# Performance work log

Measured on AMD Instinct MI355X. Metric: run time of the kernel, lower is better.

## Reference

```python
import jax, jax.numpy as jnp
import numpy as np

IN_F = 4096
OUT_F = 4096
SPLIT_F = 410   # ceil(4096 * 0.1)
NUM_PARTS = 10  # ceil(4096 / 410)


def setup_inputs() -> dict:
    key = jax.random.key(0)
    ks = jax.random.split(key, 7)
    s = 1.0 / np.sqrt(IN_F)
    sn = 1.0 / np.sqrt(NUM_PARTS)
    return {
        'x': jax.random.normal(ks[0], (2, 2048, IN_F), dtype=jnp.float32),
        'Wsel': jax.random.uniform(ks[1], (NUM_PARTS, IN_F), jnp.float32, -s, s),
        'bsel': jax.random.uniform(ks[2], (NUM_PARTS,), jnp.float32, -s, s),
        'Wexp': jax.random.uniform(ks[3], (IN_F, NUM_PARTS), jnp.float32, -sn, sn),
        'bexp': jax.random.uniform(ks[4], (IN_F,), jnp.float32, -sn, sn),
        'Wfc': jax.random.uniform(ks[5], (SPLIT_F, IN_F), jnp.float32, -s, s),
        'bfc': jax.random.uniform(ks[6], (SPLIT_F,), jnp.float32, -s, s),
        'out_features': OUT_F,
    }


def reference(x, Wsel, bsel, Wexp, bexp, Wfc, bfc, out_features):
    # selector: sx[..., n]
    sx = jnp.einsum('bsi,ni->bsn', x, Wsel) + bsel
    # expander(diag_embed(sx)): px[..., n, f] = sx[..., n] * Wexp[f, n] + bexp[f]
    # (diag matrix never materialized; mathematically identical)
    px = sx[..., :, None] * Wexp.T[None, None, :, :] + bexp  # [b, s, n, in]
    xx = x[..., None, :] + px                                # broadcast-add of x
    y = jnp.einsum('bsni,fi->bsnf', xx, Wfc) + bfc           # splitfc, [b, s, n, sf]
    y = y.reshape(y.shape[0], y.shape[1], -1)                # (n sf) flatten
    return y[..., :out_features]
```

## Files before the change

### kernel.cpp

```cpp
#include <hip/hip_runtime.h>
#include <hip/hip_bf16.h>
#include <stdint.h>

#define TKS    4096
#define KD     4096
#define NSF    410
#define NPARTS 10
#define OUTF   4096

typedef unsigned short u16;
typedef __attribute__((ext_vector_type(8))) short bf16x8;
typedef __attribute__((ext_vector_type(4))) float f32x4;

#define WS_XB  0
#define WS_BSW ((size_t)TKS * KD * 2)
#define WS_SX  (WS_BSW + (size_t)448 * 512 * 8 * 2)
#define WS_GC  (WS_SX + (size_t)TKS * NPARTS * 4)

__device__ inline u16 f2bf(float f) {
    union { __hip_bfloat16 b; u16 u; } cv;
    cv.b = __float2bfloat16(f);
    return cv.u;
}

__device__ inline int g_row(int g) { int s = g >> 6; return (s >> 2) * 32 + (s & 1) * 16 + (g & 15); }
__device__ inline int g_col(int g) { int s = g >> 6; return ((s >> 1) & 1) * 32 + ((g >> 4) & 3) * 8; }

__global__ __launch_bounds__(256) void prep(const float* __restrict__ x,
                                            const float* __restrict__ Wsel,
                                            const float* __restrict__ bsel,
                                            const float* __restrict__ Wexp,
                                            const float* __restrict__ bexp,
                                            const float* __restrict__ Wfc,
                                            const float* __restrict__ bfc,
                                            u16* __restrict__ xb,
                                            u16* __restrict__ bsw,
                                            float* __restrict__ sxb,
                                            float* __restrict__ gc) {
    const int bid = blockIdx.x;
    const int tid = threadIdx.x;

    if (bid < 128) {
        const int b3 = bid;
        const int w = tid >> 6, lane = tid & 63;
        const int t0 = b3 * 32 + w * 8;
        float acc[8][NPARTS];
#pragma unroll
        for (int t = 0; t < 8; ++t)
#pragma unroll
            for (int n = 0; n < NPARTS; ++n) acc[t][n] = 0.f;

        for (int k4 = 0; k4 < 16; ++k4) {
            const int k = k4 * 256 + lane * 4;
            float4 ws[NPARTS];
#pragma unroll
            for (int n = 0; n < NPARTS; ++n)
                ws[n] = *(const float4*)&Wsel[(size_t)n * KD + k];
#pragma unroll
            for (int t = 0; t < 8; ++t) {
                float4 xv = *(const float4*)&x[(size_t)(t0 + t) * KD + k];
#pragma unroll
                for (int n = 0; n < NPARTS; ++n)
                    acc[t][n] += xv.x * ws[n].x + xv.y * ws[n].y
                               + xv.z * ws[n].z + xv.w * ws[n].w;
            }
        }
#pragma unroll
        for (int s = 1; s < 64; s <<= 1)
#pragma unroll
            for (int t = 0; t < 8; ++t)
#pragma unroll
                for (int n = 0; n < NPARTS; ++n)
                    acc[t][n] += __shfl_xor(acc[t][n], s);
        if (lane == 0) {
#pragma unroll
            for (int t = 0; t < 8; ++t)
#pragma unroll
                for (int n = 0; n < NPARTS; ++n)
                    sxb[(size_t)(t0 + t) * NPARTS + n] = acc[t][n] + bsel[n];
        }

    } else if (bid < 142) {
        const int b4 = bid - 128;
        const int w = tid >> 6, lane = tid & 63;
        const int f0 = b4 * 32 + w * 8;
        float acc[8][11];
#pragma unroll
        for (int t = 0; t < 8; ++t)
#pragma unroll
            for (int n = 0; n < 11; ++n) acc[t][n] = 0.f;

        for (int k4 = 0; k4 < 16; ++k4) {
            const int k = k4 * 256 + lane * 4;
            float we[4][11];
#pragma unroll
            for (int j = 0; j < 4; ++j) {
#pragma unroll
                for (int n = 0; n < NPARTS; ++n)
                    we[j][n] = Wexp[(size_t)(k + j) * NPARTS + n];
                we[j][10] = bexp[k + j];
            }
#pragma unroll
            for (int t = 0; t < 8; ++t) {
                const int f = f0 + t;
                float4 xv = (f < NSF) ? *(const float4*)&Wfc[(size_t)f * KD + k]
                                      : make_float4(0.f, 0.f, 0.f, 0.f);
#pragma unroll
                for (int n = 0; n < 11; ++n)
                    acc[t][n] += xv.x * we[0][n] + xv.y * we[1][n]
                               + xv.z * we[2][n] + xv.w * we[3][n];
            }
        }
#pragma unroll
        for (int s = 1; s < 64; s <<= 1)
#pragma unroll
            for (int t = 0; t < 8; ++t)
#pragma unroll
                for (int n = 0; n < 11; ++n)
                    acc[t][n] += __shfl_xor(acc[t][n], s);
        if (lane == 0) {
#pragma unroll
            for (int t = 0; t < 8; ++t) {
                const int f = f0 + t;
#pragma unroll
                for (int n = 0; n < NPARTS; ++n)
                    gc[(size_t)f * 12 + n] = (f < NSF) ? acc[t][n] : 0.f;
                gc[(size_t)f * 12 + 10] = (f < NSF) ? acc[t][10] + bfc[f] : 0.f;
            }
        }

    } else if (bid < 8334) {
        const int b1 = bid - 142;
        const int kt = b1 & 63, tb = b1 >> 6;
        const int g = tid;
        const int slot = g >> 6;
        const int row = (slot & 1) * 16 + (g & 15);
        const int col = (slot >> 1) * 32 + ((g >> 4) & 3) * 8;
        const float* src = x + (size_t)(tb * 32 + row) * KD + kt * 64 + col;
        float4 v0 = *(const float4*)src;
        float4 v1 = *(const float4*)(src + 4);
        u16 h[8] = { f2bf(v0.x), f2bf(v0.y), f2bf(v0.z), f2bf(v0.w),
                     f2bf(v1.x), f2bf(v1.y), f2bf(v1.z), f2bf(v1.w) };
        *(uint4*)&xb[((size_t)(tb * 64 + kt) * 256 + g) * 8] = *(uint4*)h;

    } else {
        const int b2 = bid - 8334;
        const int kt = b2 & 63, rb = b2 >> 6;
        u16* tout = bsw + ((size_t)(rb * 64 + kt) * 512) * 8;
#pragma unroll
        for (int j = 0; j < 2; ++j) {
            const int g = j * 256 + tid;
            const int r = rb * 64 + g_row(g);
            uint4 pk = make_uint4(0u, 0u, 0u, 0u);
            if (r < NSF) {
                const float* src = Wfc + (size_t)r * KD + kt * 64 + g_col(g);
                float4 v0 = *(const float4*)src;
                float4 v1 = *(const float4*)(src + 4);
                u16 h[8] = { f2bf(v0.x), f2bf(v0.y), f2bf(v0.z), f2bf(v0.w),
                             f2bf(v1.x), f2bf(v1.y), f2bf(v1.z), f2bf(v1.w) };
                pk = *(uint4*)h;
            }
            *(uint4*)&tout[(size_t)g * 8] = pk;
        }
    }
}

#define A_IDX(kt, mi, ks) ((((size_t)(tb * 2 + ((mi) >> 1)) * 64 + (size_t)(kt)) * 256 \
                            + ((ks) * 2 + ((mi) & 1)) * 64 + lane) * 8)
#define B_IDX(kt, nj, ks) (((size_t)(fb * 64 + (kt)) * 512 \
                            + (wf * 4 + (ks) * 2 + (nj)) * 64 + lane) * 8)

__global__ __launch_bounds__(256, 2) void main_kernel(const u16* __restrict__ xb,
                                                      const u16* __restrict__ bsw,
                                                      float* __restrict__ out) {
    __shared__ float red[4][4][16][34];

    const int tid = threadIdx.x;
    const int f2 = blockIdx.x >> 6;
    const int tb = blockIdx.x & 63;
    const int lane = tid & 63;
    const int kh = tid >> 6;
    const int q = lane >> 4, ml = lane & 15;
    const int fb = f2 >> 1, wf = f2 & 1;

    f32x4 acc[4][2];
#pragma unroll
    for (int mi = 0; mi < 4; ++mi)
#pragma unroll
        for (int nj = 0; nj < 2; ++nj) acc[mi][nj] = (f32x4){0.f,0.f,0.f,0.f};

    bf16x8 fa[4][4], fbv[4][2];

#define LOADAB(p, kt, ks) do {                                            \
        _Pragma("unroll")                                                 \
        for (int mi = 0; mi < 4; ++mi)                                    \
            fa[p][mi] = *(const bf16x8*)&xb[A_IDX((kt), mi, (ks))];       \
        _Pragma("unroll")                                                 \
        for (int nj = 0; nj < 2; ++nj)                                    \
            fbv[p][nj] = *(const bf16x8*)&bsw[B_IDX((kt), nj, (ks))];     \
    } while (0)

#define MFMAS(p) do {                                                     \
        _Pragma("unroll")                                                 \
        for (int mi = 0; mi < 4; ++mi)                                    \
            _Pragma("unroll")                                             \
            for (int nj = 0; nj < 2; ++nj)                                \
                acc[mi][nj] = __builtin_amdgcn_mfma_f32_16x16x32_bf16(    \
                    fa[p][mi], fbv[p][nj], acc[mi][nj], 0, 0, 0);         \
    } while (0)

#define LD(p, s) LOADAB((p), kh * 16 + ((s) >> 1), (s) & 1)

    LD(0, 0); LD(1, 1); LD(2, 2);
    __builtin_amdgcn_sched_group_barrier(0x020, 18, 0);
#pragma unroll
    for (int s = 0; s < 32; ++s) {
        if (s + 3 < 32) LD((s + 3) & 3, s + 3);
        MFMAS(s & 3);
        if (s + 3 < 32)
            __builtin_amdgcn_sched_group_barrier(0x020, 6, 0);
        __builtin_amdgcn_sched_group_barrier(0x008, 8, 0);
    }
#undef LD
#undef LOADAB
#undef MFMAS

#pragma unroll
    for (int mi = 0; mi < 4; ++mi)
#pragma unroll
        for (int nj = 0; nj < 2; ++nj)
#pragma unroll
            for (int r = 0; r < 4; ++r)
                red[mi][kh][q * 4 + r][nj * 16 + ml] = acc[mi][nj][r];
    __syncthreads();

#pragma unroll
    for (int nj = 0; nj < 2; ++nj) {
        const int fl = nj * 16 + ml;
        const int fg = f2 * 32 + fl;
        if (fg >= NSF) continue;
#pragma unroll
        for (int r = 0; r < 4; ++r) {
            const int tl = kh * 16 + q * 4 + r;
            const float v = red[kh][0][q * 4 + r][fl] + red[kh][1][q * 4 + r][fl]
                          + red[kh][2][q * 4 + r][fl] + red[kh][3][q * 4 + r][fl];
            out[(size_t)(tb * 64 + tl) * OUTF + fg] = v;
        }
    }
}

__global__ __launch_bounds__(256) void expand(const float* __restrict__ sxb,
                                              const float* __restrict__ gc,
                                              float* out) {
    __shared__ float Ct[4][412];
    __shared__ float sxl[4][NPARTS];
    const int tid = threadIdx.x;
    const int t0 = blockIdx.x * 4;

    int   ns[4][4], fgs[4][4];
    float gv[4][4], cv[4][4];
#pragma unroll
    for (int g = 0; g < 4; ++g)
#pragma unroll
        for (int e = 0; e < 4; ++e) {
            const int j = g * 1024 + tid * 4 + e;
            const int n = j / NSF;
            const int fg = j - n * NSF;
            ns[g][e] = n; fgs[g][e] = fg;
            gv[g][e] = gc[(size_t)fg * 12 + n];
            cv[g][e] = gc[(size_t)fg * 12 + 10];
        }

    for (int i = tid; i < 4 * NSF; i += 256)
        Ct[i / NSF][i % NSF] = out[(size_t)(t0 + i / NSF) * OUTF + (i % NSF)];
    if (tid < 4 * NPARTS)
        sxl[tid / NPARTS][tid % NPARTS] =
            sxb[(size_t)(t0 + tid / NPARTS) * NPARTS + tid % NPARTS];
    __syncthreads();

#pragma unroll
    for (int r = 0; r < 4; ++r) {
        float* orow = out + (size_t)(t0 + r) * OUTF;
#pragma unroll
        for (int g = 0; g < 4; ++g) {
            float4 v;
            v.x = Ct[r][fgs[g][0]] + sxl[r][ns[g][0]] * gv[g][0] + cv[g][0];
            v.y = Ct[r][fgs[g][1]] + sxl[r][ns[g][1]] * gv[g][1] + cv[g][1];
            v.z = Ct[r][fgs[g][2]] + sxl[r][ns[g][2]] * gv[g][2] + cv[g][2];
            v.w = Ct[r][fgs[g][3]] + sxl[r][ns[g][3]] * gv[g][3] + cv[g][3];
            *(float4*)&orow[g * 1024 + tid * 4] = v;
        }
    }
}

extern "C" void kernel_launch(void* const* d_in, const int* in_sizes, int n_in,
                              void* d_out, int out_size, void* d_ws, size_t ws_size,
                              hipStream_t stream) {
    const float* x    = (const float*)d_in[0];
    const float* Wsel = (const float*)d_in[1];
    const float* bsel = (const float*)d_in[2];
    const float* Wexp = (const float*)d_in[3];
    const float* bexp = (const float*)d_in[4];
    const float* Wfc  = (const float*)d_in[5];
    const float* bfc  = (const float*)d_in[6];
    float* out = (float*)d_out;

    char* ws = (char*)d_ws;
    u16* xb    = (u16*)(ws + WS_XB);
    u16* bsw   = (u16*)(ws + WS_BSW);
    float* sxb = (float*)(ws + WS_SX);
    float* gcv = (float*)(ws + WS_GC);

    prep<<<dim3(128 + 14 + 8192 + 448), dim3(256), 0, stream>>>(
        x, Wsel, bsel, Wexp, bexp, Wfc, bfc, xb, bsw, sxb, gcv);
    main_kernel<<<dim3(13 * 64), dim3(256), 0, stream>>>(xb, bsw, out);
    expand<<<dim3(1024), dim3(256), 0, stream>>>(sxb, gcv, out);
}
```

Baseline: 206.5 us.

## Split selector/gate reductions across K chunks with atomics into separate kernel

The long serial selector and gate-coefficient reductions, which ran as 142 blocks each looping over all of K, are split into 8 K-chunks per block group and combined with atomicAdd in a new kernel. The per-chunk results go into a buffer that the retile kernel zeroes first. The retile path now converts two K tiles per block, which halves its block count. The goal is to stop a few slow blocks from setting the tail of the prep kernel, at the cost of an extra launch, atomics and non-deterministic summation order.

New measurement: 235.4 us. 1.14x slower.

```diff
diff --git a/kernel.cpp b/kernel.cpp
--- a/kernel.cpp
+++ b/kernel.cpp
@@ -16,6 +16,7 @@
 #define WS_BSW ((size_t)TKS * KD * 2)
 #define WS_SX  (WS_BSW + (size_t)448 * 512 * 8 * 2)
 #define WS_GC  (WS_SX + (size_t)TKS * NPARTS * 4)
+#define ZERO_U4 ((TKS * NPARTS + 448 * 12) * 4 / 16)
 
 __device__ inline u16 f2bf(float f) {
     union { __hip_bfloat16 b; u16 u; } cv;
@@ -26,125 +27,34 @@
 __device__ inline int g_row(int g) { int s = g >> 6; return (s >> 2) * 32 + (s & 1) * 16 + (g & 15); }
 __device__ inline int g_col(int g) { int s = g >> 6; return ((s >> 1) & 1) * 32 + ((g >> 4) & 3) * 8; }
 
-__global__ __launch_bounds__(256) void prep(const float* __restrict__ x,
-                                            const float* __restrict__ Wsel,
-                                            const float* __restrict__ bsel,
-                                            const float* __restrict__ Wexp,
-                                            const float* __restrict__ bexp,
-                                            const float* __restrict__ Wfc,
-                                            const float* __restrict__ bfc,
-                                            u16* __restrict__ xb,
-                                            u16* __restrict__ bsw,
-                                            float* __restrict__ sxb,
-                                            float* __restrict__ gc) {
+__global__ __launch_bounds__(256) void retile(const float* __restrict__ x,
+                                              const float* __restrict__ Wfc,
+                                              u16* __restrict__ xb,
+                                              u16* __restrict__ bsw,
+                                              uint4* __restrict__ zbase) {
     const int bid = blockIdx.x;
     const int tid = threadIdx.x;
 
-    if (bid < 128) {
-        const int b3 = bid;
-        const int w = tid >> 6, lane = tid & 63;
-        const int t0 = b3 * 32 + w * 8;
-        float acc[8][NPARTS];
-#pragma unroll
-        for (int t = 0; t < 8; ++t)
-#pragma unroll
-            for (int n = 0; n < NPARTS; ++n) acc[t][n] = 0.f;
-
-        for (int k4 = 0; k4 < 16; ++k4) {
-            const int k = k4 * 256 + lane * 4;
-            float4 ws[NPARTS];
-#pragma unroll
-            for (int n = 0; n < NPARTS; ++n)
-                ws[n] = *(const float4*)&Wsel[(size_t)n * KD + k];
-#pragma unroll
-            for (int t = 0; t < 8; ++t) {
-                float4 xv = *(const float4*)&x[(size_t)(t0 + t) * KD + k];
-#pragma unroll
-                for (int n = 0; n < NPARTS; ++n)
-                    acc[t][n] += xv.x * ws[n].x + xv.y * ws[n].y
-                               + xv.z * ws[n].z + xv.w * ws[n].w;
-            }
-        }
-#pragma unroll
-        for (int s = 1; s < 64; s <<= 1)
-#pragma unroll
-            for (int t = 0; t < 8; ++t)
-#pragma unroll
-                for (int n = 0; n < NPARTS; ++n)
-                    acc[t][n] += __shfl_xor(acc[t][n], s);
-        if (lane == 0) {
-#pragma unroll
-            for (int t = 0; t < 8; ++t)
-#pragma unroll
-                for (int n = 0; n < NPARTS; ++n)
-                    sxb[(size_t)(t0 + t) * NPARTS + n] = acc[t][n] + bsel[n];
-        }
-
-    } else if (bid < 142) {
-        const int b4 = bid - 128;
-        const int w = tid >> 6, lane = tid & 63;
-        const int f0 = b4 * 32 + w * 8;
-        float acc[8][11];
-#pragma unroll
-        for (int t = 0; t < 8; ++t)
-#pragma unroll
-            for (int n = 0; n < 11; ++n) acc[t][n] = 0.f;
-
-        for (int k4 = 0; k4 < 16; ++k4) {
-            const int k = k4 * 256 + lane * 4;
-            float we[4][11];
-#pragma unroll
-            for (int j = 0; j < 4; ++j) {
-#pragma unroll
-                for (int n = 0; n < NPARTS; ++n)
-                    we[j][n] = Wexp[(size_t)(k + j) * NPARTS + n];
-                we[j][10] = bexp[k + j];
-            }
-#pragma unroll
-            for (int t = 0; t < 8; ++t) {
-                const int f = f0 + t;
-                float4 xv = (f < NSF) ? *(const float4*)&Wfc[(size_t)f * KD + k]
-                                      : make_float4(0.f, 0.f, 0.f, 0.f);
-#pragma unroll
-                for (int n = 0; n < 11; ++n)
-                    acc[t][n] += xv.x * we[0][n] + xv.y * we[1][n]
-                               + xv.z * we[2][n] + xv.w * we[3][n];
-            }
-        }
-#pragma unroll
-        for (int s = 1; s < 64; s <<= 1)
-#pragma unroll
-            for (int t = 0; t < 8; ++t)
-#pragma unroll
-                for (int n = 0; n < 11; ++n)
-                    acc[t][n] += __shfl_xor(acc[t][n], s);
-        if (lane == 0) {
-#pragma unroll
-            for (int t = 0; t < 8; ++t) {
-                const int f = f0 + t;
-#pragma unroll
-                for (int n = 0; n < NPARTS; ++n)
-                    gc[(size_t)f * 12 + n] = (f < NSF) ? acc[t][n] : 0.f;
-                gc[(size_t)f * 12 + 10] = (f < NSF) ? acc[t][10] + bfc[f] : 0.f;
-            }
-        }
-
-    } else if (bid < 8334) {
-        const int b1 = bid - 142;
-        const int kt = b1 & 63, tb = b1 >> 6;
+    if (bid < 4096) {
+        const int ktp = bid & 31, tb = bid >> 5;
         const int g = tid;
         const int slot = g >> 6;
         const int row = (slot & 1) * 16 + (g & 15);
         const int col = (slot >> 1) * 32 + ((g >> 4) & 3) * 8;
-        const float* src = x + (size_t)(tb * 32 + row) * KD + kt * 64 + col;
-        float4 v0 = *(const float4*)src;
-        float4 v1 = *(const float4*)(src + 4);
-        u16 h[8] = { f2bf(v0.x), f2bf(v0.y), f2bf(v0.z), f2bf(v0.w),
-                     f2bf(v1.x), f2bf(v1.y), f2bf(v1.z), f2bf(v1.w) };
-        *(uint4*)&xb[((size_t)(tb * 64 + kt) * 256 + g) * 8] = *(uint4*)h;
-
-    } else {
-        const int b2 = bid - 8334;
+        const float* src = x + (size_t)(tb * 32 + row) * KD + ktp * 128 + col;
+        float4 a0 = *(const float4*)src;
+        float4 a1 = *(const float4*)(src + 4);
+        float4 b0 = *(const float4*)(src + 64);
+        float4 b1 = *(const float4*)(src + 68);
+        u16 ha[8] = { f2bf(a0.x), f2bf(a0.y), f2bf(a0.z), f2bf(a0.w),
+                      f2bf(a1.x), f2bf(a1.y), f2bf(a1.z), f2bf(a1.w) };
+        u16 hb[8] = { f2bf(b0.x), f2bf(b0.y), f2bf(b0.z), f2bf(b0.w),
+                      f2bf(b1.x), f2bf(b1.y), f2bf(b1.z), f2bf(b1.w) };
+        *(uint4*)&xb[((size_t)(tb * 64 + ktp * 2 + 0) * 256 + g) * 8] = *(uint4*)ha;
+        *(uint4*)&xb[((size_t)(tb * 64 + ktp * 2 + 1) * 256 + g) * 8] = *(uint4*)hb;
+
+    } else if (bid < 4544) {
+        const int b2 = bid - 4096;
         const int kt = b2 & 63, rb = b2 >> 6;
         u16* tout = bsw + ((size_t)(rb * 64 + kt) * 512) * 8;
 #pragma unroll
@@ -162,6 +72,120 @@
             }
             *(uint4*)&tout[(size_t)g * 8] = pk;
         }
+
+    } else {
+        for (int i = tid; i < ZERO_U4; i += 256)
+            zbase[i] = make_uint4(0u, 0u, 0u, 0u);
+    }
+}
+
+__global__ __launch_bounds__(256) void selg(const float* __restrict__ x,
+                                            const float* __restrict__ Wsel,
+                                            const float* __restrict__ bsel,
+                                            const float* __restrict__ Wexp,
+                                            const float* __restrict__ bexp,
+                                            const float* __restrict__ Wfc,
+                                            const float* __restrict__ bfc,
+                                            float* __restrict__ sxb,
+                                            float* __restrict__ gc) {
+    const int bid = blockIdx.x;
+    const int tid = threadIdx.x;
+    const int w = tid >> 6, lane = tid & 63;
+
+    if (bid < 1024) {
+        const int b3 = bid >> 3, kc = bid & 7;
+        const int t0 = b3 * 32 + w * 8;
+        float acc[8][NPARTS];
+#pragma unroll
+        for (int t = 0; t < 8; ++t)
+#pragma unroll
+            for (int n = 0; n < NPARTS; ++n) acc[t][n] = 0.f;
+
+#pragma unroll
+        for (int k4 = 0; k4 < 2; ++k4) {
+            const int k = kc * 512 + k4 * 256 + lane * 4;
+            float4 ws[NPARTS];
+#pragma unroll
+            for (int n = 0; n < NPARTS; ++n)
+                ws[n] = *(const float4*)&Wsel[(size_t)n * KD + k];
+#pragma unroll
+            for (int t = 0; t < 8; ++t) {
+                float4 xv = *(const float4*)&x[(size_t)(t0 + t) * KD + k];
+#pragma unroll
+                for (int n = 0; n < NPARTS; ++n)
+                    acc[t][n] += xv.x * ws[n].x + xv.y * ws[n].y
+                               + xv.z * ws[n].z + xv.w * ws[n].w;
+            }
+        }
+#pragma unroll
+        for (int s = 1; s < 64; s <<= 1)
+#pragma unroll
+            for (int t = 0; t < 8; ++t)
+#pragma unroll
+                for (int n = 0; n < NPARTS; ++n)
+                    acc[t][n] += __shfl_xor(acc[t][n], s);
+        if (lane == 0) {
+#pragma unroll
+            for (int t = 0; t < 8; ++t)
+#pragma unroll
+                for (int n = 0; n < NPARTS; ++n) {
+                    float v = acc[t][n] + (kc == 0 ? bsel[n] : 0.f);
+                    atomicAdd(&sxb[(size_t)(t0 + t) * NPARTS + n], v);
+                }
+        }
+
+    } else {
+        const int b4 = bid - 1024;
+        const int fb = b4 >> 3, kc = b4 & 7;
+        const int f0 = fb * 32 + w * 8;
+        float acc[8][11];
+#pragma unroll
+        for (int t = 0; t < 8; ++t)
+#pragma unroll
+            for (int n = 0; n < 11; ++n) acc[t][n] = 0.f;
+
+#pragma unroll
+        for (int k4 = 0; k4 < 2; ++k4) {
+            const int k = kc * 512 + k4 * 256 + lane * 4;
+            float we[4][11];
+#pragma unroll
+            for (int j = 0; j < 4; ++j) {
+#pragma unroll
+                for (int n = 0; n < NPARTS; ++n)
+                    we[j][n] = Wexp[(size_t)(k + j) * NPARTS + n];
+                we[j][10] = bexp[k + j];
+            }
+#pragma unroll
+            for (int t = 0; t < 8; ++t) {
+                const int f = f0 + t;
+                float4 xv = (f < NSF) ? *(const float4*)&Wfc[(size_t)f * KD + k]
+                                      : make_float4(0.f, 0.f, 0.f, 0.f);
+#pragma unroll
+                for (int n = 0; n < 11; ++n)
+                    acc[t][n] += xv.x * we[0][n] + xv.y * we[1][n]
+                               + xv.z * we[2][n] + xv.w * we[3][n];
+            }
+        }
+#pragma unroll
+        for (int s = 1; s < 64; s <<= 1)
+#pragma unroll
+            for (int t = 0; t < 8; ++t)
+#pragma unroll
+                for (int n = 0; n < 11; ++n)
+                    acc[t][n] += __shfl_xor(acc[t][n], s);
+        if (lane == 0) {
+#pragma unroll
+            for (int t = 0; t < 8; ++t) {
+                const int f = f0 + t;
+                if (f < NSF) {
+#pragma unroll
+                    for (int n = 0; n < NPARTS; ++n)
+                        atomicAdd(&gc[(size_t)f * 12 + n], acc[t][n]);
+                    atomicAdd(&gc[(size_t)f * 12 + 10],
+                              acc[t][10] + (kc == 0 ? bfc[f] : 0.f));
+                }
+            }
+        }
     }
 }
 
@@ -311,8 +335,10 @@
     float* sxb = (float*)(ws + WS_SX);
     float* gcv = (float*)(ws + WS_GC);
 
-    prep<<<dim3(128 + 14 + 8192 + 448), dim3(256), 0, stream>>>(
-        x, Wsel, bsel, Wexp, bexp, Wfc, bfc, xb, bsw, sxb, gcv);
+    retile<<<dim3(4096 + 448 + 1), dim3(256), 0, stream>>>(
+        x, Wfc, xb, bsw, (uint4*)(ws + WS_SX));
+    selg<<<dim3(1024 + 112), dim3(256), 0, stream>>>(
+        x, Wsel, bsel, Wexp, bexp, Wfc, bfc, sxb, gcv);
     main_kernel<<<dim3(13 * 64), dim3(256), 0, stream>>>(xb, bsw, out);
     expand<<<dim3(1024), dim3(256), 0, stream>>>(sxb, gcv, out);
 }
```
